# Kernel optimization log

Hardware: AMD Instinct MI355X
Metric: run time of the kernel (lower is better)

The kernel has to match this reference:

```python
import jax, jax.numpy as jnp
import numpy as np

PATCH = 3
ALPHA = 0.1


def _unfold3x3(x):
    # x: [B, C, H, W] -> [B, C*9, H, W], torch F.unfold with k=3, pad=1, stride=1
    B, C, H, W = x.shape
    p = PATCH // 2
    xp = jnp.pad(x, ((0, 0), (0, 0), (p, p), (p, p)))
    shifts = [xp[:, :, i:i + H, j:j + W] for i in range(PATCH) for j in range(PATCH)]
    # torch unfold orders (C, kh, kw); ordering is irrelevant for the dot-product
    # correlation, but we match it anyway: stack kernel positions after channel.
    out = jnp.stack(shifts, axis=2)  # [B, C, 9, H, W]
    return out.reshape(B, C * PATCH * PATCH, H, W)


def setup_inputs() -> dict:
    key = jax.random.key(0)
    k1, k2 = jax.random.split(key)
    x_lab = jax.random.normal(k1, (4, 3, 64, 64), dtype=jnp.float32)
    feature = jax.random.normal(k2, (4, 64, 64, 64), dtype=jnp.float32)
    return {"x_lab": x_lab, "feature": feature}


def reference(x_lab, feature):
    # scale_factor=1 and feature already at (H, W): both interpolates are identity.
    B, _, H, W = x_lab.shape
    N = H * W
    x_ab = x_lab.reshape(B, 3, N).transpose(0, 2, 1)          # [B, N, 3]
    lf = _unfold3x3(feature).reshape(B, -1, N)                 # [B, C*9, N]
    corr = jnp.einsum('bcn,bcm->bnm', lf, lf)                  # [B, N, N]
    attn = jax.nn.softmax(corr / ALPHA, axis=-1)
    weighted = jnp.einsum('bnm,bmc->bnc', attn, x_ab)          # [B, N, 3]
    return weighted.transpose(0, 2, 1).reshape(B, 3, H, W)
```

## Files before the change

### kernel.cpp

```cpp
#include <hip/hip_runtime.h>


#define NPIX 4096
#define ROWCH 528
#define ROWB  (ROWCH * 16)
#define SCALE 10.0f
#define XCH   2048

typedef __attribute__((ext_vector_type(8))) short bf16x8;
typedef __attribute__((ext_vector_type(4))) float f32x4;

#define MF(a, b, c) __builtin_amdgcn_mfma_f32_16x16x32_bf16(a, b, c, 0, 0, 0)

__device__ __forceinline__ uint4 pack8(const float* v) {
    unsigned h[8];
#pragma unroll
    for (int j = 0; j < 8; ++j) {
        unsigned u = __float_as_uint(v[j]);
        u = u + 0x7fffu + ((u >> 16) & 1u);
        h[j] = u >> 16;
    }
    return (uint4){h[0] | (h[1] << 16), h[2] | (h[3] << 16),
                   h[4] | (h[5] << 16), h[6] | (h[7] << 16)};
}

__device__ __forceinline__ void load_row(const float* fr, int kc, int x, float* L) {
#pragma unroll
    for (int j = 0; j < 8; ++j) L[j] = fr[(size_t)(kc * 8 + j) * NPIX + x];
}

#define MG(T, DBASE, KT) do {                                                 \
    _Pragma("unroll")                                                         \
    for (int dx = 0; dx < 3; ++dx)                                            \
        _Pragma("unroll")                                                     \
        for (int ks = 0; ks < 2; ++ks)                                        \
            acc[T][KT] = MF(AF[((DBASE) + dx) * 2 + ks], B2[ks][dx], acc[T][KT]); \
} while (0)

#define RETIRE(S, myv) do {                                                   \
    _Pragma("unroll")                                                         \
    for (int kt = 0; kt < 2; ++kt) {                                          \
        const int kx = kh * 32 + kt * 16 + nl;                                \
        const float xv0 = xls[(myv) * 64 + kx];                               \
        const float xv1 = xls[XCH + (myv) * 64 + kx];                         \
        const float xv2 = xls[2 * XCH + (myv) * 64 + kx];                     \
        _Pragma("unroll")                                                     \
        for (int rg = 0; rg < 4; ++rg) {                                      \
            const float e = __expf(fmaf(acc[S][kt][rg], SCALE, negM[rg]));    \
            l_[rg] += e;                                                      \
            A0[rg] = fmaf(e, xv0, A0[rg]);                                    \
            A1[rg] = fmaf(e, xv1, A1[rg]);                                    \
            A2[rg] = fmaf(e, xv2, A2[rg]);                                    \
        }                                                                     \
        acc[S][kt] = (f32x4){0.f, 0.f, 0.f, 0.f};                             \
    }                                                                         \
} while (0)

#define STEP(RM, SN, SR, tt) do {                                             \
    const int t_ = (tt);                                                      \
    if (t_ <= 31) *(uint4*)(ring + (SR) * ROWB + wu16) = P;                   \
    if (t_ <= 30) {                                                           \
        const int g3 = K0 + 2 + t_;                                           \
        if (g3 < 64) { load_row(featb + g3 * 64, kc, x, L); P = pack8(L); }   \
        else P = (uint4){0u, 0u, 0u, 0u};                                     \
    }                                                                         \
    if (t_ <= 33) {                                                           \
        const char* base = ring + (RM) * ROWB + bu;                           \
        _Pragma("unroll")                                                     \
        for (int kt = 0; kt < 2; ++kt) {                                      \
            bf16x8 B2[2][3];                                                  \
            _Pragma("unroll")                                                 \
            for (int ks = 0; ks < 2; ++ks) {                                  \
                const char* p = base + (ks * 264 + kt * 16) * 16;             \
                B2[ks][0] = *(const bf16x8*)(p);                              \
                B2[ks][1] = *(const bf16x8*)(p + 16);                         \
                B2[ks][2] = *(const bf16x8*)(p + 32);                         \
            }                                                                 \
            if (t_ >= 2)              MG(SR, 6, kt);        \
            if (t_ >= 1 && t_ <= 32)  MG(RM, 3, kt);        \
            if (t_ <= 31)             MG(SN, 0, kt);        \
        }                                                                     \
    }                                                                         \
    if (t_ >= 2 && t_ <= 33) RETIRE(SR, t_ - 2);                              \
    if (t_ <= 33) __syncthreads();                                            \
} while (0)

__global__ __launch_bounds__(512)
__attribute__((amdgpu_waves_per_eu(2)))
void nlwa_fused(const float* __restrict__ x_lab,
                const float* __restrict__ feature,
                float4* __restrict__ ws)
{
    __shared__ __align__(16) char ring[3 * ROWB];
    __shared__ float xls[3 * XCH];
    __shared__ float part[3][8][64];
    __shared__ float ssq[3][64];
    __shared__ float4 scrF[64][2];

    const int tid = threadIdx.x;
    const int b = blockIdx.x >> 7;
    const int r7 = blockIdx.x & 127;
    const int ny = r7 >> 1, half = r7 & 1;
    const int K0 = half * 32;
    const int w = tid >> 6, lane = tid & 63;
    const int quad = lane >> 4, nl = lane & 15;
    const int qw = w & 3, kh = w >> 2;
    const int kc = w, x = lane;
    const int wu16 = (kc * 66 + x + 1) * 16;
    const int bu = (quad * 66 + kh * 32 + nl) * 16;

    const float* featb = feature + (size_t)b * 64 * NPIX;
    const float* xb = x_lab + (size_t)b * 3 * NPIX;

    {
        const int base = K0 * 64;
        float4* d4 = (float4*)xls;
        for (int i = tid; i < 3 * XCH / 4; i += 512) {
            const int ch = i >> 9, off = i & 511;
            d4[i] = *(const float4*)(xb + (size_t)ch * NPIX + base + off * 4);
        }
    }
    if (tid < 48) {
        const int sl = tid / 16, pu = tid % 16;
        const int u = (pu >> 1) * 66 + (pu & 1) * 65;
        *(uint4*)(ring + sl * ROWB + u * 16) = (uint4){0u, 0u, 0u, 0u};
    }

    float L[8];
#pragma unroll
    for (int dyi = 0; dyi < 3; ++dyi) {
        const int qr = ny + dyi - 1;
        float ss = 0.f;
        if (qr >= 0 && qr < 64) {
            load_row(featb + qr * 64, kc, x, L);
#pragma unroll
            for (int j = 0; j < 8; ++j) ss = fmaf(L[j], L[j], ss);
            *(uint4*)(ring + dyi * ROWB + wu16) = pack8(L);
        } else {
            *(uint4*)(ring + dyi * ROWB + wu16) = (uint4){0u, 0u, 0u, 0u};
        }
        part[dyi][kc][x] = ss;
    }
    __syncthreads();

    if (tid < 192) {
        const int dyi = tid >> 6, xx = tid & 63;
        float s = 0.f;
#pragma unroll
        for (int k = 0; k < 8; ++k) s += part[dyi][k][xx];
        ssq[dyi][xx] = s;
    }

    bf16x8 AF[18];
#pragma unroll
    for (int dyi = 0; dyi < 3; ++dyi)
#pragma unroll
        for (int dx = 0; dx < 3; ++dx)
#pragma unroll
            for (int ks = 0; ks < 2; ++ks)
                AF[(dyi * 3 + dx) * 2 + ks] = *(const bf16x8*)(ring + dyi * ROWB +
                    ((quad + ks * 4) * 66 + qw * 16 + nl + dx) * 16);
    __syncthreads();

    float negM[4];
#pragma unroll
    for (int rg = 0; rg < 4; ++rg) {
        const int q = qw * 16 + quad * 4 + rg;
        float a = 0.f;
#pragma unroll
        for (int dyi = 0; dyi < 3; ++dyi)
#pragma unroll
            for (int dx = -1; dx <= 1; ++dx) {
                const int cx = q + dx;
                a += (cx >= 0 && cx < 64) ? ssq[dyi][cx] : 0.f;
            }
        negM[rg] = -SCALE * a;
    }

#pragma unroll
    for (int rr = 0; rr < 2; ++rr) {
        const int g = K0 - 1 + rr;
        if (g >= 0) {
            load_row(featb + g * 64, kc, x, L);
            *(uint4*)(ring + rr * ROWB + wu16) = pack8(L);
        } else {
            *(uint4*)(ring + rr * ROWB + wu16) = (uint4){0u, 0u, 0u, 0u};
        }
    }
    load_row(featb + (K0 + 1) * 64, kc, x, L);
    uint4 P = pack8(L);

    float l_[4], A0[4], A1[4], A2[4];
#pragma unroll
    for (int rg = 0; rg < 4; ++rg) { l_[rg] = 0.f; A0[rg] = 0.f; A1[rg] = 0.f; A2[rg] = 0.f; }
    f32x4 acc[3][2];
#pragma unroll
    for (int i = 0; i < 3; ++i) {
        acc[i][0] = (f32x4){0.f, 0.f, 0.f, 0.f};
        acc[i][1] = (f32x4){0.f, 0.f, 0.f, 0.f};
    }
    __syncthreads();

    for (int rb = 0; rb < 36; rb += 3) {
        STEP(0, 1, 2, rb);
        STEP(1, 2, 0, rb + 1);
        STEP(2, 0, 1, rb + 2);
    }

#pragma unroll
    for (int rg = 0; rg < 4; ++rg) {
#pragma unroll
        for (int off = 8; off >= 1; off >>= 1) {
            l_[rg] += __shfl_down(l_[rg], off, 16);
            A0[rg] += __shfl_down(A0[rg], off, 16);
            A1[rg] += __shfl_down(A1[rg], off, 16);
            A2[rg] += __shfl_down(A2[rg], off, 16);
        }
    }
    if (nl == 0) {
#pragma unroll
        for (int rg = 0; rg < 4; ++rg) {
            const int q = qw * 16 + quad * 4 + rg;
            scrF[q][kh] = make_float4(l_[rg], A0[rg], A1[rg], A2[rg]);
        }
    }
    __syncthreads();
    if (tid < 64) {
        const float4 t0 = scrF[tid][0], t1 = scrF[tid][1];
        ws[(size_t)blockIdx.x * 64 + tid] =
            make_float4(t0.x + t1.x, t0.y + t1.y, t0.z + t1.z, t0.w + t1.w);
    }
}

__global__ __launch_bounds__(256)
void nlwa_combine(const float4* __restrict__ ws, float* __restrict__ out)
{
    const int i = blockIdx.x * 256 + threadIdx.x;
    const int b = i >> 12, ny = (i >> 6) & 63, q = i & 63;
    const float4 p0 = ws[(size_t)(((b * 64 + ny) * 2) + 0) * 64 + q];
    const float4 p1 = ws[(size_t)(((b * 64 + ny) * 2) + 1) * 64 + q];
    const float inv = 1.0f / (p0.x + p1.x);
    float* o = out + (size_t)b * 3 * NPIX + ny * 64 + q;
    o[0]        = (p0.y + p1.y) * inv;
    o[NPIX]     = (p0.z + p1.z) * inv;
    o[2 * NPIX] = (p0.w + p1.w) * inv;
}

extern "C" void kernel_launch(void* const* d_in, const int* in_sizes, int n_in,
                              void* d_out, int out_size, void* d_ws, size_t ws_size,
                              hipStream_t stream) {
    (void)in_sizes; (void)n_in; (void)out_size; (void)ws_size;
    const float* x_lab   = (const float*)d_in[0];
    const float* feature = (const float*)d_in[1];
    float* out = (float*)d_out;
    float4* ws = (float4*)d_ws;
    nlwa_fused<<<dim3(512), dim3(512), 0, stream>>>(x_lab, feature, ws);
    nlwa_combine<<<dim3(64), dim3(256), 0, stream>>>(ws, out);
}
```

Measured before the change: 153.3 us.

## Split key range into quarters with 256-thread blocks and wider per-wave key tiles

Each block now covers a quarter of the key rows (16 instead of 32) with 4 waves instead of 8. Each wave handles all 64 key columns (4 MFMA column tiles), so the cross-wave scratch reduction disappears and partials go straight to the workspace. The grid doubles to 1024 blocks and the combine kernel sums four partials per query. In exchange, the query A-fragment load and the halo-row loads are repeated in more blocks, and each wave holds more accumulator registers.

New measurement: 136.5 us. 1.12x faster.

```diff
diff --git a/kernel.cpp b/kernel.cpp
--- a/kernel.cpp
+++ b/kernel.cpp
@@ -2,10 +2,9 @@
 
 
 #define NPIX 4096
-#define ROWCH 528
-#define ROWB  (ROWCH * 16)
+#define ROWB  (528 * 16)
 #define SCALE 10.0f
-#define XCH   2048
+#define XCH   1024
 
 typedef __attribute__((ext_vector_type(8))) short bf16x8;
 typedef __attribute__((ext_vector_type(4))) float f32x4;
@@ -39,8 +38,8 @@
 
 #define RETIRE(S, myv) do {                                                   \
     _Pragma("unroll")                                                         \
-    for (int kt = 0; kt < 2; ++kt) {                                          \
-        const int kx = kh * 32 + kt * 16 + nl;                                \
+    for (int kt = 0; kt < 4; ++kt) {                                          \
+        const int kx = kt * 16 + nl;                                          \
         const float xv0 = xls[(myv) * 64 + kx];                               \
         const float xv1 = xls[XCH + (myv) * 64 + kx];                         \
         const float xv2 = xls[2 * XCH + (myv) * 64 + kx];                     \
@@ -58,16 +57,23 @@
 
 #define STEP(RM, SN, SR, tt) do {                                             \
     const int t_ = (tt);                                                      \
-    if (t_ <= 31) *(uint4*)(ring + (SR) * ROWB + wu16) = P;                   \
-    if (t_ <= 30) {                                                           \
-        const int g3 = K0 + 2 + t_;                                           \
-        if (g3 < 64) { load_row(featb + g3 * 64, kc, x, L); P = pack8(L); }   \
-        else P = (uint4){0u, 0u, 0u, 0u};                                     \
-    }                                                                         \
-    if (t_ <= 33) {                                                           \
+    if (t_ <= 15) {                                                           \
+        *(uint4*)(ring + (SR) * ROWB + wu0) = P0;                             \
+        *(uint4*)(ring + (SR) * ROWB + wu1) = P1;                             \
+    }                                                                         \
+    if (t_ <= 14) {                                                           \
+        const int g3 = R0 + 2 + t_;                                           \
+        if (g3 < 64) {                                                        \
+            load_row(featb + g3 * 64, kc0, x, L); P0 = pack8(L);              \
+            load_row(featb + g3 * 64, kc1, x, L); P1 = pack8(L);              \
+        } else {                                                              \
+            P0 = (uint4){0u, 0u, 0u, 0u}; P1 = (uint4){0u, 0u, 0u, 0u};       \
+        }                                                                     \
+    }                                                                         \
+    {                                                                         \
         const char* base = ring + (RM) * ROWB + bu;                           \
         _Pragma("unroll")                                                     \
-        for (int kt = 0; kt < 2; ++kt) {                                      \
+        for (int kt = 0; kt < 4; ++kt) {                                      \
             bf16x8 B2[2][3];                                                  \
             _Pragma("unroll")                                                 \
             for (int ks = 0; ks < 2; ++ks) {                                  \
@@ -77,15 +83,15 @@
                 B2[ks][2] = *(const bf16x8*)(p + 32);                         \
             }                                                                 \
             if (t_ >= 2)              MG(SR, 6, kt);        \
-            if (t_ >= 1 && t_ <= 32)  MG(RM, 3, kt);        \
-            if (t_ <= 31)             MG(SN, 0, kt);        \
+            if (t_ >= 1 && t_ <= 16)  MG(RM, 3, kt);        \
+            if (t_ <= 15)             MG(SN, 0, kt);        \
         }                                                                     \
     }                                                                         \
-    if (t_ >= 2 && t_ <= 33) RETIRE(SR, t_ - 2);                              \
-    if (t_ <= 33) __syncthreads();                                            \
+    if (t_ >= 2) RETIRE(SR, t_ - 2);                                          \
+    if (t_ < 17) __syncthreads();                                             \
 } while (0)
 
-__global__ __launch_bounds__(512)
+__global__ __launch_bounds__(256)
 __attribute__((amdgpu_waves_per_eu(2)))
 void nlwa_fused(const float* __restrict__ x_lab,
                 const float* __restrict__ feature,
@@ -93,30 +99,30 @@
 {
     __shared__ __align__(16) char ring[3 * ROWB];
     __shared__ float xls[3 * XCH];
-    __shared__ float part[3][8][64];
+    __shared__ float part[3][4][64];
     __shared__ float ssq[3][64];
-    __shared__ float4 scrF[64][2];
 
     const int tid = threadIdx.x;
-    const int b = blockIdx.x >> 7;
-    const int r7 = blockIdx.x & 127;
-    const int ny = r7 >> 1, half = r7 & 1;
-    const int K0 = half * 32;
+    const int b = blockIdx.x >> 8;
+    const int rem = blockIdx.x & 255;
+    const int ny = rem >> 2, kq = rem & 3;
+    const int R0 = kq * 16;
     const int w = tid >> 6, lane = tid & 63;
     const int quad = lane >> 4, nl = lane & 15;
-    const int qw = w & 3, kh = w >> 2;
-    const int kc = w, x = lane;
-    const int wu16 = (kc * 66 + x + 1) * 16;
-    const int bu = (quad * 66 + kh * 32 + nl) * 16;
+    const int kc0 = 2 * w, kc1 = 2 * w + 1;
+    const int x = lane;
+    const int wu0 = (kc0 * 66 + x + 1) * 16;
+    const int wu1 = (kc1 * 66 + x + 1) * 16;
+    const int bu = (quad * 66 + nl) * 16;
 
     const float* featb = feature + (size_t)b * 64 * NPIX;
     const float* xb = x_lab + (size_t)b * 3 * NPIX;
 
     {
-        const int base = K0 * 64;
+        const int base = R0 * 64;
         float4* d4 = (float4*)xls;
-        for (int i = tid; i < 3 * XCH / 4; i += 512) {
-            const int ch = i >> 9, off = i & 511;
+        for (int i = tid; i < 3 * XCH / 4; i += 256) {
+            const int ch = i >> 8, off = i & 255;
             d4[i] = *(const float4*)(xb + (size_t)ch * NPIX + base + off * 4);
         }
     }
@@ -132,14 +138,19 @@
         const int qr = ny + dyi - 1;
         float ss = 0.f;
         if (qr >= 0 && qr < 64) {
-            load_row(featb + qr * 64, kc, x, L);
+            load_row(featb + qr * 64, kc0, x, L);
 #pragma unroll
             for (int j = 0; j < 8; ++j) ss = fmaf(L[j], L[j], ss);
-            *(uint4*)(ring + dyi * ROWB + wu16) = pack8(L);
+            *(uint4*)(ring + dyi * ROWB + wu0) = pack8(L);
+            load_row(featb + qr * 64, kc1, x, L);
+#pragma unroll
+            for (int j = 0; j < 8; ++j) ss = fmaf(L[j], L[j], ss);
+            *(uint4*)(ring + dyi * ROWB + wu1) = pack8(L);
         } else {
-            *(uint4*)(ring + dyi * ROWB + wu16) = (uint4){0u, 0u, 0u, 0u};
-        }
-        part[dyi][kc][x] = ss;
+            *(uint4*)(ring + dyi * ROWB + wu0) = (uint4){0u, 0u, 0u, 0u};
+            *(uint4*)(ring + dyi * ROWB + wu1) = (uint4){0u, 0u, 0u, 0u};
+        }
+        part[dyi][w][x] = ss;
     }
     __syncthreads();
 
@@ -147,7 +158,7 @@
         const int dyi = tid >> 6, xx = tid & 63;
         float s = 0.f;
 #pragma unroll
-        for (int k = 0; k < 8; ++k) s += part[dyi][k][xx];
+        for (int k = 0; k < 4; ++k) s += part[dyi][k][xx];
         ssq[dyi][xx] = s;
     }
 
@@ -159,13 +170,13 @@
 #pragma unroll
             for (int ks = 0; ks < 2; ++ks)
                 AF[(dyi * 3 + dx) * 2 + ks] = *(const bf16x8*)(ring + dyi * ROWB +
-                    ((quad + ks * 4) * 66 + qw * 16 + nl + dx) * 16);
+                    ((quad + ks * 4) * 66 + w * 16 + nl + dx) * 16);
     __syncthreads();
 
     float negM[4];
 #pragma unroll
     for (int rg = 0; rg < 4; ++rg) {
-        const int q = qw * 16 + quad * 4 + rg;
+        const int q = w * 16 + quad * 4 + rg;
         float a = 0.f;
 #pragma unroll
         for (int dyi = 0; dyi < 3; ++dyi)
@@ -179,29 +190,33 @@
 
 #pragma unroll
     for (int rr = 0; rr < 2; ++rr) {
-        const int g = K0 - 1 + rr;
+        const int g = R0 - 1 + rr;
         if (g >= 0) {
-            load_row(featb + g * 64, kc, x, L);
-            *(uint4*)(ring + rr * ROWB + wu16) = pack8(L);
+            load_row(featb + g * 64, kc0, x, L);
+            *(uint4*)(ring + rr * ROWB + wu0) = pack8(L);
+            load_row(featb + g * 64, kc1, x, L);
+            *(uint4*)(ring + rr * ROWB + wu1) = pack8(L);
         } else {
-            *(uint4*)(ring + rr * ROWB + wu16) = (uint4){0u, 0u, 0u, 0u};
-        }
-    }
-    load_row(featb + (K0 + 1) * 64, kc, x, L);
-    uint4 P = pack8(L);
+            *(uint4*)(ring + rr * ROWB + wu0) = (uint4){0u, 0u, 0u, 0u};
+            *(uint4*)(ring + rr * ROWB + wu1) = (uint4){0u, 0u, 0u, 0u};
+        }
+    }
+    uint4 P0, P1;
+    load_row(featb + (R0 + 1) * 64, kc0, x, L); P0 = pack8(L);
+    load_row(featb + (R0 + 1) * 64, kc1, x, L); P1 = pack8(L);
 
     float l_[4], A0[4], A1[4], A2[4];
 #pragma unroll
     for (int rg = 0; rg < 4; ++rg) { l_[rg] = 0.f; A0[rg] = 0.f; A1[rg] = 0.f; A2[rg] = 0.f; }
-    f32x4 acc[3][2];
-#pragma unroll
-    for (int i = 0; i < 3; ++i) {
-        acc[i][0] = (f32x4){0.f, 0.f, 0.f, 0.f};
-        acc[i][1] = (f32x4){0.f, 0.f, 0.f, 0.f};
-    }
+    f32x4 acc[3][4];
+#pragma unroll
+    for (int i = 0; i < 3; ++i)
+#pragma unroll
+        for (int kt = 0; kt < 4; ++kt)
+            acc[i][kt] = (f32x4){0.f, 0.f, 0.f, 0.f};
     __syncthreads();
 
-    for (int rb = 0; rb < 36; rb += 3) {
+    for (int rb = 0; rb < 18; rb += 3) {
         STEP(0, 1, 2, rb);
         STEP(1, 2, 0, rb + 1);
         STEP(2, 0, 1, rb + 2);
@@ -220,15 +235,10 @@
     if (nl == 0) {
 #pragma unroll
         for (int rg = 0; rg < 4; ++rg) {
-            const int q = qw * 16 + quad * 4 + rg;
-            scrF[q][kh] = make_float4(l_[rg], A0[rg], A1[rg], A2[rg]);
-        }
-    }
-    __syncthreads();
-    if (tid < 64) {
-        const float4 t0 = scrF[tid][0], t1 = scrF[tid][1];
-        ws[(size_t)blockIdx.x * 64 + tid] =
-            make_float4(t0.x + t1.x, t0.y + t1.y, t0.z + t1.z, t0.w + t1.w);
+            const int q = w * 16 + quad * 4 + rg;
+            ws[(size_t)blockIdx.x * 64 + q] =
+                make_float4(l_[rg], A0[rg], A1[rg], A2[rg]);
+        }
     }
 }
 
@@ -237,13 +247,18 @@
 {
     const int i = blockIdx.x * 256 + threadIdx.x;
     const int b = i >> 12, ny = (i >> 6) & 63, q = i & 63;
-    const float4 p0 = ws[(size_t)(((b * 64 + ny) * 2) + 0) * 64 + q];
-    const float4 p1 = ws[(size_t)(((b * 64 + ny) * 2) + 1) * 64 + q];
-    const float inv = 1.0f / (p0.x + p1.x);
+    const size_t base = ((size_t)(b * 64 + ny) * 4) * 64 + q;
+    float4 s = make_float4(0.f, 0.f, 0.f, 0.f);
+#pragma unroll
+    for (int kq = 0; kq < 4; ++kq) {
+        const float4 p = ws[base + (size_t)kq * 64];
+        s.x += p.x; s.y += p.y; s.z += p.z; s.w += p.w;
+    }
+    const float inv = 1.0f / s.x;
     float* o = out + (size_t)b * 3 * NPIX + ny * 64 + q;
-    o[0]        = (p0.y + p1.y) * inv;
-    o[NPIX]     = (p0.z + p1.z) * inv;
-    o[2 * NPIX] = (p0.w + p1.w) * inv;
+    o[0]        = s.y * inv;
+    o[NPIX]     = s.z * inv;
+    o[2 * NPIX] = s.w * inv;
 }
 
 extern "C" void kernel_launch(void* const* d_in, const int* in_sizes, int n_in,
@@ -254,6 +269,6 @@
     const float* feature = (const float*)d_in[1];
     float* out = (float*)d_out;
     float4* ws = (float4*)d_ws;
-    nlwa_fused<<<dim3(512), dim3(512), 0, stream>>>(x_lab, feature, ws);
+    nlwa_fused<<<dim3(1024), dim3(256), 0, stream>>>(x_lab, feature, ws);
     nlwa_combine<<<dim3(64), dim3(256), 0, stream>>>(ws, out);
 }
```
